# Kernel tuning notes

Hardware: AMD Instinct MI355X
Metric: run time of the kernel (lower is better)

The kernel has to match this reference:

```python
import jax, jax.numpy as jnp
import numpy as np

N_NODES = 50000
DROP_P = 0.25


def gcn_conv(x, edge_index, W, b, n_nodes):
    """PyG GCNConv: symmetric-normalized aggregation with self-loops.
    out = D^{-1/2} (A + I) D^{-1/2} (x @ W) + b
    """
    E = edge_index.shape[1]
    loops = jnp.arange(n_nodes, dtype=edge_index.dtype)
    src = jnp.concatenate([edge_index[0], loops])  # [E+N]
    dst = jnp.concatenate([edge_index[1], loops])  # [E+N]

    h = x @ W  # [N, out] dense GEMM

    ones = jnp.ones(E + n_nodes, dtype=x.dtype)
    deg = jax.ops.segment_sum(ones, dst, num_segments=n_nodes)  # [N]
    dinv = jnp.where(deg > 0, jax.lax.rsqrt(deg), 0.0)
    norm = dinv[src] * dinv[dst]  # [E+N]

    msgs = h[src] * norm[:, None]  # gather + scale, [E+N, out]
    out = jax.ops.segment_sum(msgs, dst, num_segments=n_nodes)  # scatter-add
    return out + b


def reference(x, edge_index, W1, b1, W2, b2):
    n = x.shape[0]
    h = gcn_conv(x, edge_index, W1, b1, n)
    h = jax.nn.elu(h)
    # F.dropout(p=0.25) defaults to training=True -> active dropout with
    # inverted scaling; deterministic mask from a fixed key.
    keep = jax.random.bernoulli(jax.random.key(42), 1.0 - DROP_P, h.shape)
    h = jnp.where(keep, h / (1.0 - DROP_P), 0.0).astype(h.dtype)
    out = gcn_conv(h, edge_index, W2, b2, n)
    return out


def setup_inputs() -> dict:
    key = jax.random.key(0)
    k1, k2, k3, k4 = jax.random.split(key, 4)
    C = 512
    E = 800000
    x = jax.random.normal(k1, (N_NODES, C), dtype=jnp.float32)
    edge_index = jax.random.randint(k2, (2, E), 0, N_NODES, dtype=jnp.int64)
    # Glorot-style scaled weights
    W1 = jax.random.normal(k3, (C, C // 2), dtype=jnp.float32) * (1.0 / np.sqrt(C))
    b1 = jnp.zeros((C // 2,), dtype=jnp.float32)
    W2 = jax.random.normal(k4, (C // 2, 1), dtype=jnp.float32) * (1.0 / np.sqrt(C // 2))
    b2 = jnp.zeros((1,), dtype=jnp.float32)
    return {"x": x, "edge_index": edge_index, "W1": W1, "b1": b1, "W2": W2, "b2": b2}
```

## Files before the change

### kernel.cpp

```cpp
#include <hip/hip_runtime.h>
#include <stdint.h>


typedef float floatx4 __attribute__((ext_vector_type(4)));
typedef _Float16 f16;
typedef _Float16 f16x8 __attribute__((ext_vector_type(8)));

union F16x8 {
  f16x8 v;
  f16 e[8];
  uint4 q;
};

__device__ __forceinline__ void tf_round(uint32_t& x0, uint32_t& x1, int r) {
  x0 += x1;
  x1 = (x1 << r) | (x1 >> (32 - r));
  x1 ^= x0;
}

__device__ __forceinline__ void threefry_0_42(uint32_t c0, uint32_t c1,
                                              uint32_t& o0, uint32_t& o1) {
  const uint32_t ks0 = 0u;
  const uint32_t ks1 = 42u;
  const uint32_t ks2 = 0x1BD11BDAu ^ 0u ^ 42u;
  uint32_t x0 = c0 + ks0;
  uint32_t x1 = c1 + ks1;
  tf_round(x0, x1, 13); tf_round(x0, x1, 15); tf_round(x0, x1, 26); tf_round(x0, x1, 6);
  x0 += ks1; x1 += ks2 + 1u;
  tf_round(x0, x1, 17); tf_round(x0, x1, 29); tf_round(x0, x1, 16); tf_round(x0, x1, 24);
  x0 += ks2; x1 += ks0 + 2u;
  tf_round(x0, x1, 13); tf_round(x0, x1, 15); tf_round(x0, x1, 26); tf_round(x0, x1, 6);
  x0 += ks0; x1 += ks1 + 3u;
  tf_round(x0, x1, 17); tf_round(x0, x1, 29); tf_round(x0, x1, 16); tf_round(x0, x1, 24);
  x0 += ks1; x1 += ks2 + 4u;
  tf_round(x0, x1, 13); tf_round(x0, x1, 15); tf_round(x0, x1, 26); tf_round(x0, x1, 6);
  x0 += ks2; x1 += ks0 + 5u;
  o0 = x0; o1 = x1;
}

__global__ void k_deg(const int* __restrict__ dst, int E, int* __restrict__ deg) {
  int e = blockIdx.x * blockDim.x + threadIdx.x;
  if (e < E) atomicAdd(&deg[dst[e]], 1);
}

__global__ __launch_bounds__(256) void k_scan1(const int* __restrict__ deg,
                                               int* __restrict__ excl,
                                               int* __restrict__ sums,
                                               float* __restrict__ dinv, int N) {
  __shared__ int sm[256];
  int tid = threadIdx.x;
  int i = blockIdx.x * 256 + tid;
  int v = (i < N) ? deg[i] : 0;
  if (i < N) dinv[i] = 1.0f / sqrtf((float)(v + 1));
  sm[tid] = v;
  __syncthreads();
#pragma unroll
  for (int off = 1; off < 256; off <<= 1) {
    int t = (tid >= off) ? sm[tid - off] : 0;
    __syncthreads();
    sm[tid] += t;
    __syncthreads();
  }
  if (i < N) excl[i] = sm[tid] - v;
  if (tid == 255) sums[blockIdx.x] = sm[255];
}

__global__ __launch_bounds__(1024) void k_scan2(int* __restrict__ sums, int nb) {
  __shared__ int sm[1024];
  int tid = threadIdx.x;
  int v = (tid < nb) ? sums[tid] : 0;
  sm[tid] = v;
  __syncthreads();
#pragma unroll
  for (int off = 1; off < 1024; off <<= 1) {
    int t = (tid >= off) ? sm[tid - off] : 0;
    __syncthreads();
    sm[tid] += t;
    __syncthreads();
  }
  if (tid < nb) sums[tid] = sm[tid] - v;
}

__global__ void k_scan3(int* __restrict__ rowptr, int* __restrict__ cursor,
                        const int* __restrict__ sums, int N, int E) {
  int i = blockIdx.x * blockDim.x + threadIdx.x;
  if (i < N) {
    int r = rowptr[i] + sums[i >> 8];
    rowptr[i] = r;
    cursor[i] = r;
  }
  if (i == 0) rowptr[N] = E;
}

__global__ void k_bucket(const int* __restrict__ src, const int* __restrict__ dst,
                         int* __restrict__ cursor, int* __restrict__ csr_src, int E) {
  int e = blockIdx.x * blockDim.x + threadIdx.x;
  if (e < E) {
    int pos = atomicAdd(&cursor[dst[e]], 1);
    csr_src[pos] = src[e];
  }
}

__global__ void k_prep_w1t(const float* __restrict__ W1,
                           f16* __restrict__ Bpk) {
  int t = blockIdx.x * blockDim.x + threadIdx.x;
  if (t >= 512 * 256) return;
  int k = t >> 8, n = t & 255;
  int ks = k >> 5, quad = (k >> 3) & 3, j = k & 7;
  int nt = n >> 4, lane = quad * 16 + (n & 15);
  size_t e = ((size_t)(ks * 16 + nt)) * 64 + lane;
  Bpk[e * 8 + j] = (f16)W1[t];
}

__global__ __launch_bounds__(256) void k_gemm_mfma(
    const float* __restrict__ A,
    const uint4* __restrict__ Bpk,
    const float* __restrict__ dinv,
    f16* __restrict__ C,
    int M) {
  __shared__ f16 As[2][64 * 40];
  const int tid = threadIdx.x;
  const int cg = tid >> 6;
  const int lane = tid & 63;
  const int quad = lane >> 4;
  const int l16 = lane & 15;
  const int m0 = blockIdx.x * 64;

  const int srow = tid >> 2;
  const int scq = tid & 3;
  int grow = m0 + srow;
  if (grow >= M) grow = M - 1;
  const float* gsp = A + (size_t)grow * 512 + scq * 8;
  f16* lwp = &As[0][srow * 40 + scq * 8];
  const int lstride = 64 * 40;

  auto cvt8 = [](float4 a, float4 b) {
    F16x8 r;
    r.e[0] = (f16)a.x; r.e[1] = (f16)a.y; r.e[2] = (f16)a.z; r.e[3] = (f16)a.w;
    r.e[4] = (f16)b.x; r.e[5] = (f16)b.y; r.e[6] = (f16)b.z; r.e[7] = (f16)b.w;
    return r;
  };

  {
    float4 s0 = *(const float4*)(gsp);
    float4 s1 = *(const float4*)(gsp + 4);
    *(uint4*)lwp = cvt8(s0, s1).q;
  }
  __syncthreads();

  floatx4 acc[4][4];
#pragma unroll
  for (int fr = 0; fr < 4; ++fr)
#pragma unroll
    for (int t = 0; t < 4; ++t) acc[fr][t] = (floatx4){0.f, 0.f, 0.f, 0.f};

  const uint4* bp0 = Bpk + lane + (size_t)(cg * 4) * 64;

  for (int ks = 0; ks < 16; ++ks) {
    const int cur = ks & 1;
    const int nxt = cur ^ 1;

    float4 p0, p1;
    if (ks < 15) {
      p0 = *(const float4*)(gsp + (ks + 1) * 32);
      p1 = *(const float4*)(gsp + (ks + 1) * 32 + 4);
    }

    const uint4* bp = bp0 + (size_t)ks * 1024;
    F16x8 bfrag[4];
#pragma unroll
    for (int t = 0; t < 4; ++t) bfrag[t].q = bp[t * 64];

#pragma unroll
    for (int fr = 0; fr < 4; ++fr) {
      F16x8 af;
      af.q = *(const uint4*)&As[cur][(fr * 16 + l16) * 40 + quad * 8];
#pragma unroll
      for (int t = 0; t < 4; ++t) {
        acc[fr][t] = __builtin_amdgcn_mfma_f32_16x16x32_f16(af.v, bfrag[t].v, acc[fr][t], 0, 0, 0);
      }
    }

    if (ks < 15) {
      *(uint4*)(lwp + nxt * lstride) = cvt8(p0, p1).q;
    }
    __syncthreads();
  }

#pragma unroll
  for (int fr = 0; fr < 4; ++fr)
#pragma unroll
    for (int r = 0; r < 4; ++r) {
      int gm = m0 + fr * 16 + quad * 4 + r;
      if (gm < M) {
        float dv = dinv[gm];
#pragma unroll
        for (int t = 0; t < 4; ++t) {
          const int col = (cg * 4 + t) * 16 + l16;
          C[(size_t)gm * 256 + col] = (f16)(dv * acc[fr][t][r]);
        }
      }
    }
}

__global__ __launch_bounds__(256) void k_gather_fused(
    const int* __restrict__ rowptr, const int* __restrict__ csr_src,
    const float* __restrict__ dinv, const f16* __restrict__ hs,
    const float* __restrict__ b1, const float* __restrict__ W2,
    float* __restrict__ zs, int N) {
  int wave = (blockIdx.x * blockDim.x + threadIdx.x) >> 6;
  int lane = threadIdx.x & 63;
  int half = lane >> 5;
  int l = lane & 31;
  int d = wave * 2 + half;
  bool valid = d < N;
  if (!valid) d = N - 1;
  float dd = dinv[d];
  int beg = rowptr[d], end = rowptr[d + 1];
  int f0 = l << 3;

  float acc[8];
  {
    F16x8 hv;
    hv.q = *(const uint4*)(hs + ((size_t)d << 8) + f0);
#pragma unroll
    for (int i = 0; i < 8; ++i) acc[i] = (float)hv.e[i];
  }

  int e = beg;
  for (; e + 3 < end; e += 4) {
    int s0 = csr_src[e], s1 = csr_src[e + 1], s2 = csr_src[e + 2], s3 = csr_src[e + 3];
    F16x8 a, b, c, dq;
    a.q = *(const uint4*)(hs + ((size_t)s0 << 8) + f0);
    b.q = *(const uint4*)(hs + ((size_t)s1 << 8) + f0);
    c.q = *(const uint4*)(hs + ((size_t)s2 << 8) + f0);
    dq.q = *(const uint4*)(hs + ((size_t)s3 << 8) + f0);
#pragma unroll
    for (int i = 0; i < 8; ++i)
      acc[i] += (float)a.e[i] + (float)b.e[i] + (float)c.e[i] + (float)dq.e[i];
  }
  for (; e < end; ++e) {
    int s0 = csr_src[e];
    F16x8 a;
    a.q = *(const uint4*)(hs + ((size_t)s0 << 8) + f0);
#pragma unroll
    for (int i = 0; i < 8; ++i) acc[i] += (float)a.e[i];
  }

  float4 bb0 = *(const float4*)(b1 + f0);
  float4 bb1 = *(const float4*)(b1 + f0 + 4);
  float4 w0  = *(const float4*)(W2 + f0);
  float4 w1  = *(const float4*)(W2 + f0 + 4);
  const float* bbp[8] = {&bb0.x, &bb0.y, &bb0.z, &bb0.w, &bb1.x, &bb1.y, &bb1.z, &bb1.w};
  const float* wp[8]  = {&w0.x, &w0.y, &w0.z, &w0.w, &w1.x, &w1.y, &w1.z, &w1.w};

  float sum = 0.f;
  uint32_t jbase = ((uint32_t)d << 8) + (uint32_t)f0;
#pragma unroll
  for (int i = 0; i < 8; ++i) {
    uint32_t r0, r1;
    threefry_0_42(0u, jbase + i, r0, r1);
    uint32_t bits = r0 ^ r1;
    float u = __uint_as_float((bits >> 9) | 0x3f800000u) - 1.0f;
    float va = dd * acc[i] + *bbp[i];
    float ea = va > 0.f ? va : expm1f(va);
    float ha = (u < 0.75f) ? (ea * (1.0f / 0.75f)) : 0.f;
    sum += ha * *wp[i];
  }
#pragma unroll
  for (int off = 16; off > 0; off >>= 1) sum += __shfl_down(sum, off, 32);
  if (l == 0 && valid) zs[d] = dd * sum;
}

__global__ __launch_bounds__(256) void k_gather2(
    const int* __restrict__ rowptr, const int* __restrict__ csr_src,
    const float* __restrict__ dinv, const float* __restrict__ zs,
    const float* __restrict__ b2, float* __restrict__ out, int N) {
  int wave = (blockIdx.x * blockDim.x + threadIdx.x) >> 6;
  int lane = threadIdx.x & 63;
  int sub = lane >> 4;
  int l = lane & 15;
  int d = wave * 4 + sub;
  bool valid = d < N;
  if (!valid) d = N - 1;
  float dd = dinv[d];
  int beg = rowptr[d], end = rowptr[d + 1];

  float acc = 0.f;
  for (int e = beg + l; e < end; e += 16) {
    acc += zs[csr_src[e]];
  }
#pragma unroll
  for (int off = 8; off > 0; off >>= 1) acc += __shfl_down(acc, off, 16);
  if (l == 0 && valid) out[d] = b2[0] + dd * (zs[d] + acc);
}

extern "C" void kernel_launch(void* const* d_in, const int* in_sizes, int n_in,
                              void* d_out, int out_size, void* d_ws, size_t ws_size,
                              hipStream_t stream) {
  const float* x  = (const float*)d_in[0];
  const int*   ei = (const int*)d_in[1];
  const float* W1 = (const float*)d_in[2];
  const float* b1 = (const float*)d_in[3];
  const float* W2 = (const float*)d_in[4];
  const float* b2 = (const float*)d_in[5];
  float* out = (float*)d_out;

  const int E = in_sizes[1] / 2;
  const int N = in_sizes[0] / 512;
  const int* src = ei;
  const int* dst = ei + E;

  char* ws = (char*)d_ws;
  size_t off = 0;
  auto alloc = [&](size_t bytes) -> void* {
    void* p = ws + off;
    off += (bytes + 255) & ~(size_t)255;
    return p;
  };
  int*   deg     = (int*)  alloc((size_t)N * 4);
  int*   rowptr  = (int*)  alloc((size_t)(N + 1) * 4);
  int*   cursor  = (int*)  alloc((size_t)N * 4);
  int*   csr_src = (int*)  alloc((size_t)E * 4);
  int*   sums    = (int*)  alloc(1024 * 4);
  float* dinv    = (float*)alloc((size_t)N * 4);
  f16*   hs      = (f16*)  alloc((size_t)N * 256 * 2);
  float* zs      = (float*)alloc((size_t)N * 4);
  f16*   Bpk     = (f16*)  alloc(512 * 256 * 2);

  const int nb = (N + 255) / 256;

  hipMemsetAsync(deg, 0, (size_t)N * 4, stream);
  k_prep_w1t<<<(512 * 256 + 255) / 256, 256, 0, stream>>>(W1, Bpk);
  k_deg<<<(E + 255) / 256, 256, 0, stream>>>(dst, E, deg);
  k_scan1<<<nb, 256, 0, stream>>>(deg, rowptr, sums, dinv, N);
  k_scan2<<<1, 1024, 0, stream>>>(sums, nb);
  k_scan3<<<(N + 255) / 256, 256, 0, stream>>>(rowptr, cursor, sums, N, E);
  k_bucket<<<(E + 255) / 256, 256, 0, stream>>>(src, dst, cursor, csr_src, E);

  k_gemm_mfma<<<(N + 63) / 64, 256, 0, stream>>>(x, (const uint4*)Bpk, dinv, hs, N);

  const int nwaves1 = (N + 1) / 2;
  k_gather_fused<<<(nwaves1 * 64 + 255) / 256, 256, 0, stream>>>(rowptr, csr_src, dinv, hs,
                                                                 b1, W2, zs, N);
  const int nwaves2 = (N + 3) / 4;
  k_gather2<<<(nwaves2 * 64 + 255) / 256, 256, 0, stream>>>(rowptr, csr_src, dinv, zs, b2, out, N);
}
```

Before: 357.2 us.

## Precompute dropout bitmask in graph-build kernels; accumulate gather in packed fp16

The Threefry dropout mask is now computed as a packed bitmask, one byte per 8 features. Those threads are piggybacked onto the atomic-bound degree and bucketing kernels, so the fused gather only loads a byte instead of running 8 Threefry hashes per lane. The gather now accumulates neighbour rows in packed fp16 vector adds instead of converting to fp32. It loads the CSR indices as aligned int4 after a peel loop, and uses __expf-1 instead of expm1f. fp16 accumulation over roughly 17 neighbours risks precision loss and overflow. The extra 1.6 MB mask buffer adds memory traffic.

```diff
diff --git a/kernel.cpp b/kernel.cpp
--- a/kernel.cpp
+++ b/kernel.cpp
@@ -38,9 +38,24 @@
   o0 = x0; o1 = x1;
 }
 
-__global__ void k_deg(const int* __restrict__ dst, int E, int* __restrict__ deg) {
-  int e = blockIdx.x * blockDim.x + threadIdx.x;
-  if (e < E) atomicAdd(&deg[dst[e]], 1);
+__device__ __forceinline__ unsigned char mask_byte(uint32_t b) {
+  uint32_t jb = b << 3;
+  uint32_t m = 0;
+#pragma unroll
+  for (int i = 0; i < 8; ++i) {
+    uint32_t r0, r1;
+    threefry_0_42(0u, jb + (uint32_t)i, r0, r1);
+    uint32_t bits = r0 ^ r1;
+    m |= (bits < 0xC0000000u ? 1u : 0u) << i;
+  }
+  return (unsigned char)m;
+}
+
+__global__ void k_deg(const int* __restrict__ dst, int E, int* __restrict__ deg,
+                      unsigned char* __restrict__ maskb, int nb0) {
+  int t = blockIdx.x * blockDim.x + threadIdx.x;
+  if (t < E) atomicAdd(&deg[dst[t]], 1);
+  if (t < nb0) maskb[t] = mask_byte((uint32_t)t);
 }
 
 __global__ __launch_bounds__(256) void k_scan1(const int* __restrict__ deg,
@@ -93,12 +108,14 @@
 }
 
 __global__ void k_bucket(const int* __restrict__ src, const int* __restrict__ dst,
-                         int* __restrict__ cursor, int* __restrict__ csr_src, int E) {
-  int e = blockIdx.x * blockDim.x + threadIdx.x;
-  if (e < E) {
-    int pos = atomicAdd(&cursor[dst[e]], 1);
-    csr_src[pos] = src[e];
-  }
+                         int* __restrict__ cursor, int* __restrict__ csr_src, int E,
+                         unsigned char* __restrict__ maskb, int nb0, int nb1) {
+  int t = blockIdx.x * blockDim.x + threadIdx.x;
+  if (t < E) {
+    int pos = atomicAdd(&cursor[dst[t]], 1);
+    csr_src[pos] = src[t];
+  }
+  if (t < nb1) maskb[nb0 + t] = mask_byte((uint32_t)(nb0 + t));
 }
 
 __global__ void k_prep_w1t(const float* __restrict__ W1,
@@ -207,6 +224,7 @@
     const int* __restrict__ rowptr, const int* __restrict__ csr_src,
     const float* __restrict__ dinv, const f16* __restrict__ hs,
     const float* __restrict__ b1, const float* __restrict__ W2,
+    const unsigned char* __restrict__ maskb,
     float* __restrict__ zs, int N) {
   int wave = (blockIdx.x * blockDim.x + threadIdx.x) >> 6;
   int lane = threadIdx.x & 63;
@@ -219,33 +237,37 @@
   int beg = rowptr[d], end = rowptr[d + 1];
   int f0 = l << 3;
 
-  float acc[8];
+  F16x8 accu;
+  accu.q = *(const uint4*)(hs + ((size_t)d << 8) + f0);
+  f16x8 accv = accu.v;
+
+  int e = beg;
   {
-    F16x8 hv;
-    hv.q = *(const uint4*)(hs + ((size_t)d << 8) + f0);
-#pragma unroll
-    for (int i = 0; i < 8; ++i) acc[i] = (float)hv.e[i];
-  }
-
-  int e = beg;
+    int pe = beg + ((4 - (beg & 3)) & 3);
+    if (pe > end) pe = end;
+    for (; e < pe; ++e) {
+      F16x8 a;
+      a.q = *(const uint4*)(hs + ((size_t)csr_src[e] << 8) + f0);
+      accv = accv + a.v;
+    }
+  }
   for (; e + 3 < end; e += 4) {
-    int s0 = csr_src[e], s1 = csr_src[e + 1], s2 = csr_src[e + 2], s3 = csr_src[e + 3];
+    int4 s4 = *(const int4*)(csr_src + e);
     F16x8 a, b, c, dq;
-    a.q = *(const uint4*)(hs + ((size_t)s0 << 8) + f0);
-    b.q = *(const uint4*)(hs + ((size_t)s1 << 8) + f0);
-    c.q = *(const uint4*)(hs + ((size_t)s2 << 8) + f0);
-    dq.q = *(const uint4*)(hs + ((size_t)s3 << 8) + f0);
-#pragma unroll
-    for (int i = 0; i < 8; ++i)
-      acc[i] += (float)a.e[i] + (float)b.e[i] + (float)c.e[i] + (float)dq.e[i];
+    a.q  = *(const uint4*)(hs + ((size_t)s4.x << 8) + f0);
+    b.q  = *(const uint4*)(hs + ((size_t)s4.y << 8) + f0);
+    c.q  = *(const uint4*)(hs + ((size_t)s4.z << 8) + f0);
+    dq.q = *(const uint4*)(hs + ((size_t)s4.w << 8) + f0);
+    f16x8 t0 = a.v + b.v;
+    f16x8 t1 = c.v + dq.v;
+    accv = accv + (t0 + t1);
   }
   for (; e < end; ++e) {
-    int s0 = csr_src[e];
     F16x8 a;
-    a.q = *(const uint4*)(hs + ((size_t)s0 << 8) + f0);
-#pragma unroll
-    for (int i = 0; i < 8; ++i) acc[i] += (float)a.e[i];
-  }
+    a.q = *(const uint4*)(hs + ((size_t)csr_src[e] << 8) + f0);
+    accv = accv + a.v;
+  }
+  accu.v = accv;
 
   float4 bb0 = *(const float4*)(b1 + f0);
   float4 bb1 = *(const float4*)(b1 + f0 + 4);
@@ -254,17 +276,14 @@
   const float* bbp[8] = {&bb0.x, &bb0.y, &bb0.z, &bb0.w, &bb1.x, &bb1.y, &bb1.z, &bb1.w};
   const float* wp[8]  = {&w0.x, &w0.y, &w0.z, &w0.w, &w1.x, &w1.y, &w1.z, &w1.w};
 
+  uint32_t mb = maskb[(size_t)d * 32 + l];
+
   float sum = 0.f;
-  uint32_t jbase = ((uint32_t)d << 8) + (uint32_t)f0;
 #pragma unroll
   for (int i = 0; i < 8; ++i) {
-    uint32_t r0, r1;
-    threefry_0_42(0u, jbase + i, r0, r1);
-    uint32_t bits = r0 ^ r1;
-    float u = __uint_as_float((bits >> 9) | 0x3f800000u) - 1.0f;
-    float va = dd * acc[i] + *bbp[i];
-    float ea = va > 0.f ? va : expm1f(va);
-    float ha = (u < 0.75f) ? (ea * (1.0f / 0.75f)) : 0.f;
+    float va = dd * (float)accu.e[i] + *bbp[i];
+    float ea = va > 0.f ? va : (__expf(va) - 1.0f);
+    float ha = ((mb >> i) & 1u) ? (ea * (1.0f / 0.75f)) : 0.f;
     sum += ha * *wp[i];
   }
 #pragma unroll
@@ -327,22 +346,30 @@
   f16*   hs      = (f16*)  alloc((size_t)N * 256 * 2);
   float* zs      = (float*)alloc((size_t)N * 4);
   f16*   Bpk     = (f16*)  alloc(512 * 256 * 2);
+  unsigned char* maskb = (unsigned char*)alloc((size_t)N * 32);
 
   const int nb = (N + 255) / 256;
+
+  const int nbytes = N * 32;
+  const int nb0 = nbytes >> 1;
+  const int nb1 = nbytes - nb0;
+  const int tdeg = (E > nb0) ? E : nb0;
+  const int tbkt = (E > nb1) ? E : nb1;
 
   hipMemsetAsync(deg, 0, (size_t)N * 4, stream);
   k_prep_w1t<<<(512 * 256 + 255) / 256, 256, 0, stream>>>(W1, Bpk);
-  k_deg<<<(E + 255) / 256, 256, 0, stream>>>(dst, E, deg);
+  k_deg<<<(tdeg + 255) / 256, 256, 0, stream>>>(dst, E, deg, maskb, nb0);
   k_scan1<<<nb, 256, 0, stream>>>(deg, rowptr, sums, dinv, N);
   k_scan2<<<1, 1024, 0, stream>>>(sums, nb);
   k_scan3<<<(N + 255) / 256, 256, 0, stream>>>(rowptr, cursor, sums, N, E);
-  k_bucket<<<(E + 255) / 256, 256, 0, stream>>>(src, dst, cursor, csr_src, E);
+  k_bucket<<<(tbkt + 255) / 256, 256, 0, stream>>>(src, dst, cursor, csr_src, E,
+                                                   maskb, nb0, nb1);
 
   k_gemm_mfma<<<(N + 63) / 64, 256, 0, stream>>>(x, (const uint4*)Bpk, dinv, hs, N);
 
   const int nwaves1 = (N + 1) / 2;
   k_gather_fused<<<(nwaves1 * 64 + 255) / 256, 256, 0, stream>>>(rowptr, csr_src, dinv, hs,
-                                                                 b1, W2, zs, N);
+                                                                 b1, W2, maskb, zs, N);
   const int nwaves2 = (N + 3) / 4;
   k_gather2<<<(nwaves2 * 64 + 255) / 256, 256, 0, stream>>>(rowptr, csr_src, dinv, zs, b2, out, N);
 }
```

Measured after the change: 345.6 us. 1.03x faster.
